# Optimization experiments

Measured on AMD Instinct MI355X. Metric: run time of the kernel, lower is better.

Reference implementation:

```python
import jax, jax.numpy as jnp
import numpy as np

T, N, F, H, C = 32, 20000, 128, 128, 10
LN_EPS = 1e-5


def setup_inputs() -> dict:
    key = jax.random.key(0)
    ks = jax.random.split(key, 11)
    u = lambda k, shp, bound: jax.random.uniform(k, shp, jnp.float32, -bound, bound)
    bh = 1.0 / np.sqrt(H)  # torch RNNCell / Linear init scale
    return {
        "X": jax.random.normal(ks[0], (T, N, F), jnp.float32),
        "W_ih": u(ks[1], (H, F), bh),
        "W_hh": u(ks[2], (H, H), bh),
        "b_ih": u(ks[3], (H,), bh),
        "b_hh": u(ks[4], (H,), bh),
        "ln_gamma": jnp.ones((H,), jnp.float32),
        "ln_beta": jnp.zeros((H,), jnp.float32),
        "attn_W": u(ks[5], (1, H), bh),
        "attn_b": u(ks[6], (1,), bh),
        "dense_W": u(ks[7], (C, H), bh),
        "dense_b": u(ks[8], (C,), bh),
    }


def reference(X, W_ih, W_hh, b_ih, b_hh, ln_gamma, ln_beta, attn_W, attn_b, dense_W, dense_b):
    # --- R: initial hidden (no ReLU, as in source init branch) ---
    h0 = X[0] @ W_ih.T + b_hh + b_ih  # (N, H)

    def step(h, x):
        h_new = jax.nn.relu(x @ W_ih.T + b_ih + h @ W_hh.T + b_hh)
        return h_new, h_new

    _, outs = jax.lax.scan(step, h0, X)  # (T, N, H)

    # LayerNorm over last dim (dropout is identity in eval / p=0)
    mu = jnp.mean(outs, axis=-1, keepdims=True)
    var = jnp.var(outs, axis=-1, keepdims=True)
    outs = (outs - mu) * jax.lax.rsqrt(var + LN_EPS) * ln_gamma + ln_beta

    # --- attn: linear -> softmax over time axis 0 ---
    a = jax.nn.softmax(outs @ attn_W.T + attn_b, axis=0)  # (T, N, 1)

    # --- dense: linear -> weight by attention -> sum over time ---
    d = outs @ dense_W.T + dense_b  # (T, N, C)
    return jnp.sum(d * a, axis=0)  # (N, C)
```

## Files before the change

kernel.cpp:

```cpp
#include <hip/hip_runtime.h>
#include <math.h>

#define TT 32
#define NN 20000
#define FF 128
#define HH 128
#define CC 10
#define RPB 32
#define NTHREADS 512

typedef __attribute__((ext_vector_type(8))) _Float16 f16x8;
typedef __attribute__((ext_vector_type(4))) _Float16 f16x4;
typedef __attribute__((ext_vector_type(4))) float f32x4;

#define PLANE_LO 16384
#define Y_OFF    32768
#define WS_LO    32768
#define WS_D     65536
#define A_ADDR(row, chunk) (((row) << 9) + ((((chunk) ^ ((row) & 15))) << 4))
#define Y_ADDR(row, chunk) (Y_OFF + ((row) << 8) + ((((chunk) ^ ((row) & 15))) << 4))

__device__ __forceinline__ void split8(float4 a, float4 b, f16x8* hi, f16x8* lo) {
    float v[8] = {a.x, a.y, a.z, a.w, b.x, b.y, b.z, b.w};
    f16x8 h, l;
#pragma unroll
    for (int j = 0; j < 8; ++j) {
        _Float16 hh = (_Float16)v[j];
        h[j] = hh;
        l[j] = (_Float16)(v[j] - (float)hh);
    }
    *hi = h; *lo = l;
}

__global__ __launch_bounds__(256, 1)
void grn_prep(const float* __restrict__ W_ih,
              const float* __restrict__ W_hh,
              const float* __restrict__ dense_W,
              const float* __restrict__ attn_w,
              _Float16* __restrict__ wsg)
{
    const int i  = blockIdx.x * 256 + threadIdx.x;
    const int kg = i & 31;
    const int c  = i >> 5;
    const int k0 = kg << 3;
    const float* src = (k0 < 128) ? (W_ih + c * 128 + k0)
                                  : (W_hh + c * 128 + (k0 - 128));
    float4 w0 = *(const float4*)src;
    float4 w1 = *(const float4*)(src + 4);
    f16x8 whi, wlo;
    split8(w0, w1, &whi, &wlo);
    *(f16x8*)(wsg + kg * 1024 + c * 8)         = whi;
    *(f16x8*)(wsg + WS_LO + kg * 1024 + c * 8) = wlo;

    if (i < 256) {
        const int kg2 = i >> 4;
        const int cc  = i & 15;
        f16x8 d;
#pragma unroll
        for (int j = 0; j < 8; ++j) {
            const int k = (kg2 << 3) + j;
            float v = 0.f;
            if (cc < 10)       v = dense_W[cc * 128 + k];
            else if (cc == 10) v = attn_w[k];
            d[j] = (_Float16)v;
        }
        *(f16x8*)(wsg + WS_D + kg2 * 128 + cc * 8) = d;
    }
}

__global__ __launch_bounds__(NTHREADS, 1)
void grn_r14(const float* __restrict__ X,
             const _Float16* __restrict__ wsg,
             const float* __restrict__ b_ih,
             const float* __restrict__ b_hh,
             const float* __restrict__ gamma,
             const float* __restrict__ beta,
             const float* __restrict__ dense_b,
             float* __restrict__ out)
{
    __shared__ __align__(16) char smem[40960];
    char* smA = smem;

    const int tid  = threadIdx.x;
    const int lane = tid & 63;
    const int wave = tid >> 6;
    const int wm   = wave >> 2;
    const int wn   = wave & 3;
    const int n0   = blockIdx.x * RPB;

    f16x8 Whi[8][2], Wlo[8][2];
#pragma unroll
    for (int ks = 0; ks < 8; ++ks) {
        const int kc = (ks << 2) + (lane >> 4);
#pragma unroll
        for (int nt = 0; nt < 2; ++nt) {
            const int c = (wn << 5) + (nt << 4) + (lane & 15);
            Whi[ks][nt] = *(const f16x8*)(wsg + kc * 1024 + c * 8);
            Wlo[ks][nt] = *(const f16x8*)(wsg + WS_LO + kc * 1024 + c * 8);
        }
    }

    f16x8 wd[4];
    {
        const int cc = lane & 15;
#pragma unroll
        for (int ks = 0; ks < 4; ++ks) {
            const int kc = (ks << 2) + (lane >> 4);
            wd[ks] = *(const f16x8*)(wsg + WS_D + kc * 128 + cc * 8);
        }
    }

    f32x4 bias4[2];
    int kch[2], c0off[2];
#pragma unroll
    for (int nt = 0; nt < 2; ++nt) {
        const int c0 = (wn << 5) + (nt << 4) + ((lane >> 4) << 2);
        float4 bi = *(const float4*)(b_ih + c0);
        float4 bh = *(const float4*)(b_hh + c0);
        bias4[nt][0] = bi.x + bh.x; bias4[nt][1] = bi.y + bh.y;
        bias4[nt][2] = bi.z + bh.z; bias4[nt][3] = bi.w + bh.w;
        kch[nt]   = 16 + (c0 >> 3);
        c0off[nt] = (c0 & 4) << 1;
    }

    const int lrow = tid >> 4;
    const int lc   = tid & 15;
    float g[8], bb[8];
    {
        const int cb = lc << 3;
        float4 g0 = *(const float4*)(gamma + cb);
        float4 g1 = *(const float4*)(gamma + cb + 4);
        float4 b0 = *(const float4*)(beta  + cb);
        float4 b1 = *(const float4*)(beta  + cb + 4);
        g[0]=g0.x; g[1]=g0.y; g[2]=g0.z; g[3]=g0.w;
        g[4]=g1.x; g[5]=g1.y; g[6]=g1.z; g[7]=g1.w;
        bb[0]=b0.x; bb[1]=b0.y; bb[2]=b0.z; bb[3]=b0.w;
        bb[4]=b1.x; bb[5]=b1.y; bb[6]=b1.z; bb[7]=b1.w;
    }

    {
        const float* xs0 = X + (size_t)(n0 + lrow) * FF + (lc << 3);
        float4 p0 = *(const float4*)xs0;
        float4 p1 = *(const float4*)(xs0 + 4);
        f16x8 hi, lo;
        split8(p0, p1, &hi, &lo);
        *(f16x8*)(smA + A_ADDR(lrow, lc)) = hi;
        *(f16x8*)(smA + PLANE_LO + A_ADDR(lrow, lc)) = lo;
        f16x8 z;
#pragma unroll
        for (int j = 0; j < 8; ++j) z[j] = (_Float16)0.f;
        for (int i = tid; i < 1024; i += NTHREADS) {
            const int pl  = i >> 9;
            const int row = (i >> 4) & 31;
            const int ch  = 16 + (i & 15);
            *(f16x8*)(smA + pl * PLANE_LO + (row << 9) + (ch << 4)) = z;
        }
    }
    __syncthreads();

    const int rowA = (wm << 4) + (lane & 15);

    {
        f32x4 acc[2];
        acc[0] = (f32x4){0.f,0.f,0.f,0.f};
        acc[1] = (f32x4){0.f,0.f,0.f,0.f};
#pragma unroll
        for (int ks = 0; ks < 8; ++ks) {
            const int kc = (ks << 2) + (lane >> 4);
            f16x8 ah = *(const f16x8*)(smA + A_ADDR(rowA, kc));
            f16x8 al = *(const f16x8*)(smA + PLANE_LO + A_ADDR(rowA, kc));
#pragma unroll
            for (int nt = 0; nt < 2; ++nt) {
                acc[nt] = __builtin_amdgcn_mfma_f32_16x16x32_f16(Whi[ks][nt], ah, acc[nt], 0, 0, 0);
                acc[nt] = __builtin_amdgcn_mfma_f32_16x16x32_f16(Whi[ks][nt], al, acc[nt], 0, 0, 0);
                acc[nt] = __builtin_amdgcn_mfma_f32_16x16x32_f16(Wlo[ks][nt], ah, acc[nt], 0, 0, 0);
            }
        }
        __syncthreads();
#pragma unroll
        for (int nt = 0; nt < 2; ++nt) {
            f16x4 hi4, lo4;
#pragma unroll
            for (int q = 0; q < 4; ++q) {
                const float v = acc[nt][q] + bias4[nt][q];
                _Float16 hh = (_Float16)v;
                hi4[q] = hh;
                lo4[q] = (_Float16)(v - (float)hh);
            }
            const int addr = (rowA << 9) + (((kch[nt] ^ (rowA & 15))) << 4) + c0off[nt];
            *(f16x4*)(smA + addr) = hi4;
            *(f16x4*)(smA + PLANE_LO + addr) = lo4;
        }
    }
    __syncthreads();

    float stm[4], stz[4], sta[4];
#pragma unroll
    for (int s = 0; s < 4; ++s) { stm[s] = -INFINITY; stz[s] = 0.f; sta[s] = 0.f; }

    for (int t = 0; t < TT; ++t) {
        float4 p0, p1;
        if (t < TT - 1) {
            const float* xs0 = X + ((size_t)(t + 1) * NN + n0 + lrow) * FF + (lc << 3);
            p0 = *(const float4*)xs0;
            p1 = *(const float4*)(xs0 + 4);
        }

        f32x4 acc[2];
        acc[0] = (f32x4){0.f,0.f,0.f,0.f};
        acc[1] = (f32x4){0.f,0.f,0.f,0.f};
#pragma unroll
        for (int ks = 0; ks < 8; ++ks) {
            const int kc = (ks << 2) + (lane >> 4);
            f16x8 ah = *(const f16x8*)(smA + A_ADDR(rowA, kc));
            f16x8 al = *(const f16x8*)(smA + PLANE_LO + A_ADDR(rowA, kc));
#pragma unroll
            for (int nt = 0; nt < 2; ++nt) {
                acc[nt] = __builtin_amdgcn_mfma_f32_16x16x32_f16(Whi[ks][nt], ah, acc[nt], 0, 0, 0);
                acc[nt] = __builtin_amdgcn_mfma_f32_16x16x32_f16(Whi[ks][nt], al, acc[nt], 0, 0, 0);
                acc[nt] = __builtin_amdgcn_mfma_f32_16x16x32_f16(Wlo[ks][nt], ah, acc[nt], 0, 0, 0);
            }
        }
        __syncthreads();

#pragma unroll
        for (int nt = 0; nt < 2; ++nt) {
            f16x4 hi4, lo4;
#pragma unroll
            for (int q = 0; q < 4; ++q) {
                const float v = fmaxf(acc[nt][q] + bias4[nt][q], 0.f);
                _Float16 hh = (_Float16)v;
                hi4[q] = hh;
                lo4[q] = (_Float16)(v - (float)hh);
            }
            const int addr = (rowA << 9) + (((kch[nt] ^ (rowA & 15))) << 4) + c0off[nt];
            *(f16x4*)(smA + addr) = hi4;
            *(f16x4*)(smA + PLANE_LO + addr) = lo4;
        }
        if (t < TT - 1) {
            f16x8 hi, lo;
            split8(p0, p1, &hi, &lo);
            *(f16x8*)(smA + A_ADDR(lrow, lc)) = hi;
            *(f16x8*)(smA + PLANE_LO + A_ADDR(lrow, lc)) = lo;
        }
        __syncthreads();

        {
            f16x8 hv = *(const f16x8*)(smA + A_ADDR(lrow, 16 + lc));
            float v[8];
            float s1 = 0.f, s2 = 0.f;
#pragma unroll
            for (int j = 0; j < 8; ++j) { v[j] = (float)hv[j]; }
#pragma unroll
            for (int j = 0; j < 8; ++j) { s1 += v[j]; s2 += v[j] * v[j]; }
            s1 += __shfl_xor(s1, 1); s2 += __shfl_xor(s2, 1);
            s1 += __shfl_xor(s1, 2); s2 += __shfl_xor(s2, 2);
            s1 += __shfl_xor(s1, 4); s2 += __shfl_xor(s2, 4);
            s1 += __shfl_xor(s1, 8); s2 += __shfl_xor(s2, 8);
            const float mu  = s1 * (1.f / 128.f);
            const float var = s2 * (1.f / 128.f) - mu * mu;
            const float rsi = rsqrtf(var + 1e-5f);
            f16x8 y;
#pragma unroll
            for (int j = 0; j < 8; ++j)
                y[j] = (_Float16)((v[j] - mu) * rsi * g[j] + bb[j]);
            *(f16x8*)(smem + Y_ADDR(lrow, lc)) = y;
        }
        __syncthreads();

        if (wave < 2) {
            f32x4 acc2 = (f32x4){0.f,0.f,0.f,0.f};
#pragma unroll
            for (int ks = 0; ks < 4; ++ks) {
                const int kc = (ks << 2) + (lane >> 4);
                f16x8 a = *(const f16x8*)(smem + Y_ADDR((wave << 4) + (lane & 15), kc));
                acc2 = __builtin_amdgcn_mfma_f32_16x16x32_f16(a, wd[ks], acc2, 0, 0, 0);
            }
#pragma unroll
            for (int r = 0; r < 4; ++r) {
                const float dval = acc2[r];
                const float lg = __shfl(dval, (lane & 48) + 10);
                const float mn = fmaxf(stm[r], lg);
                const float sc = __expf(stm[r] - mn);
                const float e  = __expf(lg - mn);
                stz[r] = stz[r] * sc + e;
                sta[r] = sta[r] * sc + e * dval;
                stm[r] = mn;
            }
        }
    }

    if (wave < 2) {
        const int c = lane & 15;
        if (c < CC) {
            const float db = dense_b[c];
#pragma unroll
            for (int r = 0; r < 4; ++r) {
                const int row = (wave << 4) + ((lane >> 4) << 2) + r;
                out[(size_t)(n0 + row) * CC + c] = sta[r] / stz[r] + db;
            }
        }
    }
}

extern "C" void kernel_launch(void* const* d_in, const int* in_sizes, int n_in,
                              void* d_out, int out_size, void* d_ws, size_t ws_size,
                              hipStream_t stream) {
    const float* X      = (const float*)d_in[0];
    const float* W_ih   = (const float*)d_in[1];
    const float* W_hh   = (const float*)d_in[2];
    const float* b_ih   = (const float*)d_in[3];
    const float* b_hh   = (const float*)d_in[4];
    const float* gamma  = (const float*)d_in[5];
    const float* beta   = (const float*)d_in[6];
    const float* attn_w = (const float*)d_in[7];
    const float* dW     = (const float*)d_in[9];
    const float* db     = (const float*)d_in[10];
    float* out = (float*)d_out;
    _Float16* wsg = (_Float16*)d_ws;
    (void)in_sizes; (void)n_in; (void)out_size; (void)ws_size;

    grn_prep<<<dim3(16), dim3(256), 0, stream>>>(W_ih, W_hh, dW, attn_w, wsg);
    grn_r14<<<dim3(NN / RPB), dim3(NTHREADS), 0, stream>>>(
        X, wsg, b_ih, b_hh, gamma, beta, db, out);
}
```

Before: 203.6 us.

## Fuse LayerNorm into dense MFMA operand build, dropping Y smem and barrier

LayerNorm is now computed by the two MFMA waves directly in registers. Each lane loads the four h chunks that form its MFMA A-operand, reduces the row statistics with two cross-lane shuffles, and builds the normalized f16 operand in place. This removes the Y staging buffer in shared memory, one __syncthreads per timestep, and the LDS write/read round trip. The cost is that the LN work moves from all 8 waves onto 2, which lengthens the serial tail while the other waves sit idle. Gamma and beta are now kept as f16, a small precision change.

```diff
diff --git a/kernel.cpp b/kernel.cpp
--- a/kernel.cpp
+++ b/kernel.cpp
@@ -14,11 +14,9 @@
 typedef __attribute__((ext_vector_type(4))) float f32x4;
 
 #define PLANE_LO 16384
-#define Y_OFF    32768
 #define WS_LO    32768
 #define WS_D     65536
 #define A_ADDR(row, chunk) (((row) << 9) + ((((chunk) ^ ((row) & 15))) << 4))
-#define Y_ADDR(row, chunk) (Y_OFF + ((row) << 8) + ((((chunk) ^ ((row) & 15))) << 4))
 
 __device__ __forceinline__ void split8(float4 a, float4 b, f16x8* hi, f16x8* lo) {
     float v[8] = {a.x, a.y, a.z, a.w, b.x, b.y, b.z, b.w};
@@ -69,7 +67,7 @@
 }
 
 __global__ __launch_bounds__(NTHREADS, 1)
-void grn_r14(const float* __restrict__ X,
+void grn_r15(const float* __restrict__ X,
              const _Float16* __restrict__ wsg,
              const float* __restrict__ b_ih,
              const float* __restrict__ b_hh,
@@ -78,7 +76,7 @@
              const float* __restrict__ dense_b,
              float* __restrict__ out)
 {
-    __shared__ __align__(16) char smem[40960];
+    __shared__ __align__(16) char smem[32768];
     char* smA = smem;
 
     const int tid  = threadIdx.x;
@@ -107,6 +105,25 @@
         for (int ks = 0; ks < 4; ++ks) {
             const int kc = (ks << 2) + (lane >> 4);
             wd[ks] = *(const f16x8*)(wsg + WS_D + kc * 128 + cc * 8);
+        }
+    }
+
+    f16x8 gf[4], bf[4];
+    {
+        const int q = lane >> 4;
+#pragma unroll
+        for (int c = 0; c < 4; ++c) {
+            const int base = ((c << 2) + q) << 3;
+            float4 g0 = *(const float4*)(gamma + base);
+            float4 g1 = *(const float4*)(gamma + base + 4);
+            float4 b0 = *(const float4*)(beta  + base);
+            float4 b1 = *(const float4*)(beta  + base + 4);
+            f16x8 gg, bb2;
+            gg[0]=(_Float16)g0.x; gg[1]=(_Float16)g0.y; gg[2]=(_Float16)g0.z; gg[3]=(_Float16)g0.w;
+            gg[4]=(_Float16)g1.x; gg[5]=(_Float16)g1.y; gg[6]=(_Float16)g1.z; gg[7]=(_Float16)g1.w;
+            bb2[0]=(_Float16)b0.x; bb2[1]=(_Float16)b0.y; bb2[2]=(_Float16)b0.z; bb2[3]=(_Float16)b0.w;
+            bb2[4]=(_Float16)b1.x; bb2[5]=(_Float16)b1.y; bb2[6]=(_Float16)b1.z; bb2[7]=(_Float16)b1.w;
+            gf[c] = gg; bf[c] = bb2;
         }
     }
 
@@ -125,18 +142,6 @@
 
     const int lrow = tid >> 4;
     const int lc   = tid & 15;
-    float g[8], bb[8];
-    {
-        const int cb = lc << 3;
-        float4 g0 = *(const float4*)(gamma + cb);
-        float4 g1 = *(const float4*)(gamma + cb + 4);
-        float4 b0 = *(const float4*)(beta  + cb);
-        float4 b1 = *(const float4*)(beta  + cb + 4);
-        g[0]=g0.x; g[1]=g0.y; g[2]=g0.z; g[3]=g0.w;
-        g[4]=g1.x; g[5]=g1.y; g[6]=g1.z; g[7]=g1.w;
-        bb[0]=b0.x; bb[1]=b0.y; bb[2]=b0.z; bb[3]=b0.w;
-        bb[4]=b1.x; bb[5]=b1.y; bb[6]=b1.z; bb[7]=b1.w;
-    }
 
     {
         const float* xs0 = X + (size_t)(n0 + lrow) * FF + (lc << 3);
@@ -245,36 +250,37 @@
         }
         __syncthreads();
 
-        {
-            f16x8 hv = *(const f16x8*)(smA + A_ADDR(lrow, 16 + lc));
-            float v[8];
+        if (wave < 2) {
+            const int q    = lane >> 4;
+            const int rowY = (wave << 4) + (lane & 15);
+            f16x8 hv[4];
+#pragma unroll
+            for (int c = 0; c < 4; ++c)
+                hv[c] = *(const f16x8*)(smA + A_ADDR(rowY, 16 + (c << 2) + q));
+            float v[32];
             float s1 = 0.f, s2 = 0.f;
 #pragma unroll
-            for (int j = 0; j < 8; ++j) { v[j] = (float)hv[j]; }
-#pragma unroll
-            for (int j = 0; j < 8; ++j) { s1 += v[j]; s2 += v[j] * v[j]; }
-            s1 += __shfl_xor(s1, 1); s2 += __shfl_xor(s2, 1);
-            s1 += __shfl_xor(s1, 2); s2 += __shfl_xor(s2, 2);
-            s1 += __shfl_xor(s1, 4); s2 += __shfl_xor(s2, 4);
-            s1 += __shfl_xor(s1, 8); s2 += __shfl_xor(s2, 8);
+            for (int c = 0; c < 4; ++c)
+#pragma unroll
+                for (int j = 0; j < 8; ++j) {
+                    const float x = (float)hv[c][j];
+                    v[c * 8 + j] = x; s1 += x; s2 += x * x;
+                }
+            s1 += __shfl_xor(s1, 16); s2 += __shfl_xor(s2, 16);
+            s1 += __shfl_xor(s1, 32); s2 += __shfl_xor(s2, 32);
             const float mu  = s1 * (1.f / 128.f);
             const float var = s2 * (1.f / 128.f) - mu * mu;
             const float rsi = rsqrtf(var + 1e-5f);
-            f16x8 y;
-#pragma unroll
-            for (int j = 0; j < 8; ++j)
-                y[j] = (_Float16)((v[j] - mu) * rsi * g[j] + bb[j]);
-            *(f16x8*)(smem + Y_ADDR(lrow, lc)) = y;
-        }
-        __syncthreads();
-
-        if (wave < 2) {
+
             f32x4 acc2 = (f32x4){0.f,0.f,0.f,0.f};
 #pragma unroll
-            for (int ks = 0; ks < 4; ++ks) {
-                const int kc = (ks << 2) + (lane >> 4);
-                f16x8 a = *(const f16x8*)(smem + Y_ADDR((wave << 4) + (lane & 15), kc));
-                acc2 = __builtin_amdgcn_mfma_f32_16x16x32_f16(a, wd[ks], acc2, 0, 0, 0);
+            for (int c = 0; c < 4; ++c) {
+                f16x8 yf;
+#pragma unroll
+                for (int j = 0; j < 8; ++j)
+                    yf[j] = (_Float16)((v[c * 8 + j] - mu) * rsi * (float)gf[c][j]
+                                       + (float)bf[c][j]);
+                acc2 = __builtin_amdgcn_mfma_f32_16x16x32_f16(yf, wd[c], acc2, 0, 0, 0);
             }
 #pragma unroll
             for (int r = 0; r < 4; ++r) {
@@ -321,6 +327,6 @@
     (void)in_sizes; (void)n_in; (void)out_size; (void)ws_size;
 
     grn_prep<<<dim3(16), dim3(256), 0, stream>>>(W_ih, W_hh, dW, attn_w, wsg);
-    grn_r14<<<dim3(NN / RPB), dim3(NTHREADS), 0, stream>>>(
+    grn_r15<<<dim3(NN / RPB), dim3(NTHREADS), 0, stream>>>(
         X, wsg, b_ih, b_hh, gamma, beta, db, out);
 }
```

Result: slower. 359.5 us (+76.6%).
